# Kernel tuning notes

Measured on AMD Instinct MI355X. Metric: run time of the kernel, lower is better.

Reference implementation:

```python
import jax, jax.numpy as jnp
import numpy as np

N = 200000          # nodes
E = 800000          # edges (avg degree ~4, molecular graphs)
F_IN = 128          # dataset.num_node_features
HID = 32            # hidden_channels -> widths 32, 64, 128
N_TASKS = 128       # dataset.num_tasks
G = 8000            # number of graphs in the batch
EPS = 1e-5


def _glorot(key, shape):
    fan_in, fan_out = shape[0], shape[1]
    lim = np.sqrt(6.0 / (fan_in + fan_out)).astype(np.float32)
    return jax.random.uniform(key, shape, jnp.float32, -lim, lim)


def setup_inputs() -> dict:
    key = jax.random.key(0)
    ks = jax.random.split(key, 16)
    x = jax.random.normal(ks[0], (N, F_IN), jnp.float32)
    edge_index = jax.random.randint(ks[1], (2, E), 0, N, jnp.int64)
    batch = jnp.sort(jax.random.randint(ks[2], (N,), 0, G, jnp.int64))
    return {
        "x": x,
        "edge_index": edge_index,
        "batch": batch,
        "norm_w": jnp.ones((1,), jnp.float32),
        "norm_b": jnp.zeros((1,), jnp.float32),
        "W1": _glorot(ks[3], (F_IN, HID)),
        "b1": jnp.zeros((HID,), jnp.float32),
        "W2": _glorot(ks[4], (HID, 2 * HID)),
        "b2": jnp.zeros((2 * HID,), jnp.float32),
        "W3": _glorot(ks[5], (2 * HID, 4 * HID)),
        "b3": jnp.zeros((4 * HID,), jnp.float32),
        "lin1_W": _glorot(ks[6], (4 * HID, 256)),
        "lin1_b": jnp.zeros((256,), jnp.float32),
        "lin2_W": _glorot(ks[7], (256, N_TASKS)),
        "lin2_b": jnp.zeros((N_TASKS,), jnp.float32),
    }


def _instance_norm(x, batch, w, b):
    # PyG InstanceNorm: per-graph, per-channel mean / biased var, scalar affine.
    ones = jnp.ones((x.shape[0], 1), x.dtype)
    cnt = jnp.maximum(jax.ops.segment_sum(ones, batch, num_segments=G), 1.0)  # [G,1]
    mean = jax.ops.segment_sum(x, batch, num_segments=G) / cnt               # [G,C]
    var = jax.ops.segment_sum(x * x, batch, num_segments=G) / cnt - mean * mean
    xn = (x - mean[batch]) * jax.lax.rsqrt(var[batch] + EPS)
    return xn * w + b


def _gcn_conv(x, src, dst, dis, W, b):
    # GCNConv: h = xW; out_i = sum_j (d_i d_j)^{-1/2} h_j over A+I edges; + bias.
    h = x @ W
    msg = h[src] * (dis[src] * dis[dst])[:, None]          # [E, C] gather
    agg = jax.ops.segment_sum(msg, dst, num_segments=x.shape[0])
    agg = agg + h * (dis * dis)[:, None]                   # self-loop term
    return agg + b


def reference(x, edge_index, batch, norm_w, norm_b, W1, b1, W2, b2, W3, b3,
              lin1_W, lin1_b, lin2_W, lin2_b):
    src, dst = edge_index[0], edge_index[1]
    # degrees on A + I (all edge weights 1)
    deg = 1.0 + jax.ops.segment_sum(jnp.ones((E,), x.dtype), dst, num_segments=N)
    dis = jax.lax.rsqrt(deg)                                # deg >= 1, safe

    h = _instance_norm(x, batch, norm_w, norm_b)
    h = jax.nn.relu(_gcn_conv(h, src, dst, dis, W1, b1))
    h = jax.nn.relu(_gcn_conv(h, src, dst, dis, W2, b2))
    h = jax.nn.relu(_gcn_conv(h, src, dst, dis, W3, b3))

    # global_max_pool; empty graphs -> 0 (values are >=0 post-relu)
    pooled = jnp.maximum(jax.ops.segment_max(h, batch, num_segments=G), 0.0)

    out = jax.nn.relu(pooled @ lin1_W + lin1_b)
    return out @ lin2_W + lin2_b
```

## Files before the change

### kernel.cpp

```cpp
#include <hip/hip_runtime.h>
#include <hip/hip_bf16.h>
#include <stdint.h>

#define NN 200000
#define NE 800000
#define FIN 128
#define NG 8000
#define EPSV 1e-5f
#define NBS ((NN + 255) / 256)

typedef __attribute__((ext_vector_type(8))) short bf16x8;
typedef __attribute__((ext_vector_type(4))) float f32x4;

static __device__ __forceinline__ bf16x8 as_bf16x8(uint4 u) {
    union { uint4 u; bf16x8 v; } c; c.u = u; return c.v;
}

static __device__ __forceinline__ void u2f(uint4 v, float4& lo, float4& hi) {
    lo.x = __uint_as_float(v.x << 16); lo.y = __uint_as_float(v.x & 0xffff0000u);
    lo.z = __uint_as_float(v.y << 16); lo.w = __uint_as_float(v.y & 0xffff0000u);
    hi.x = __uint_as_float(v.z << 16); hi.y = __uint_as_float(v.z & 0xffff0000u);
    hi.z = __uint_as_float(v.w << 16); hi.w = __uint_as_float(v.w & 0xffff0000u);
}
static __device__ __forceinline__ unsigned int pk(float a, float b) {
    __hip_bfloat16 x = __float2bfloat16(a), y = __float2bfloat16(b);
    return (unsigned int)(*(unsigned short*)&x) | ((unsigned int)(*(unsigned short*)&y) << 16);
}

__global__ void k_cnt(const int* __restrict__ dst, int* __restrict__ cnt) {
    int e = blockIdx.x * 256 + threadIdx.x;
    if (e < NE) atomicAdd(&cnt[dst[e]], 1);
}

__global__ void k_blocksum(const int* __restrict__ cnt, int* __restrict__ bsum) {
    __shared__ int sh[256];
    int b = blockIdx.x, t = threadIdx.x;
    int idx = b * 256 + t;
    sh[t] = (idx < NN) ? cnt[idx] : 0;
    __syncthreads();
    for (int o = 128; o > 0; o >>= 1) {
        if (t < o) sh[t] += sh[t + o];
        __syncthreads();
    }
    if (t == 0) bsum[b] = sh[0];
}

__global__ __launch_bounds__(1024) void k_scanb(const int* __restrict__ bsum, int* __restrict__ bpre) {
    __shared__ int sh[1024];
    int t = threadIdx.x;
    int v = (t < NBS) ? bsum[t] : 0;
    sh[t] = v;
    __syncthreads();
    for (int o = 1; o < 1024; o <<= 1) {
        int add = (t >= o) ? sh[t - o] : 0;
        __syncthreads();
        sh[t] += add;
        __syncthreads();
    }
    if (t < NBS) bpre[t] = sh[t] - v;
}

__global__ void k_scanchunk(int* __restrict__ cnt, const int* __restrict__ bpre,
                            int* __restrict__ rowstart, int* __restrict__ cursor) {
    __shared__ int sh[256];
    int b = blockIdx.x, t = threadIdx.x;
    int idx = b * 256 + t;
    int v = (idx < NN) ? cnt[idx] : 0;
    sh[t] = v;
    __syncthreads();
    for (int o = 1; o < 256; o <<= 1) {
        int add = (t >= o) ? sh[t - o] : 0;
        __syncthreads();
        sh[t] += add;
        __syncthreads();
    }
    if (idx < NN) {
        int rs = bpre[b] + sh[t] - v;
        rowstart[idx] = rs;
        cursor[idx] = rs;
        ((float*)cnt)[idx] = rsqrtf(1.0f + (float)v);
    }
    if (idx == 0) rowstart[NN] = NE;
}

__global__ void k_fill(const int* __restrict__ src, const int* __restrict__ dst,
                       int* __restrict__ cursor, int* __restrict__ csr) {
    int e = blockIdx.x * 256 + threadIdx.x;
    if (e < NE) {
        int pos = atomicAdd(&cursor[dst[e]], 1);
        csr[pos] = src[e];
    }
}

__global__ void k_starts(const int* __restrict__ batch, int* __restrict__ startg) {
    int n = blockIdx.x * 256 + threadIdx.x;
    if (n >= NN) return;
    int b = batch[n];
    int prev = (n == 0) ? -1 : batch[n - 1];
    for (int g = prev + 1; g <= b; ++g) startg[g] = n;
    if (n == NN - 1) {
        for (int g = b + 1; g <= NG; ++g) startg[g] = NN;
    }
}

__global__ __launch_bounds__(256) void k_w3split(const float* __restrict__ W3,
                                                 unsigned short* __restrict__ whi,
                                                 unsigned short* __restrict__ wlo) {
    int i = blockIdx.x * 256 + threadIdx.x;
    if (i >= 64 * 128) return;
    int n = i >> 6, k = i & 63;
    float w = W3[k * 128 + n];
    __hip_bfloat16 h = __float2bfloat16(w);
    float hf = __bfloat162float(h);
    __hip_bfloat16 l = __float2bfloat16(w - hf);
    whi[n * 64 + k] = *(unsigned short*)&h;
    wlo[n * 64 + k] = *(unsigned short*)&l;
}

__global__ __launch_bounds__(256) void k_stats2(const float* __restrict__ x,
                                                const int* __restrict__ startg,
                                                const float* __restrict__ nw,
                                                const float* __restrict__ nb,
                                                float* __restrict__ scale,
                                                float* __restrict__ shift) {
    __shared__ float4 rsum[256], rsq[256];
    int g = blockIdx.x;
    int s = startg[g], e = startg[g + 1];
    if (s == e) return;
    int t = threadIdx.x;
    int slot = t >> 5, c4 = t & 31;
    const float4* x4 = (const float4*)x;
    float4 sum = {0.f, 0.f, 0.f, 0.f}, sq = {0.f, 0.f, 0.f, 0.f};
    for (int n = s + slot; n < e; n += 8) {
        float4 v = x4[n * 32 + c4];
        sum.x += v.x; sum.y += v.y; sum.z += v.z; sum.w += v.w;
        sq.x += v.x * v.x; sq.y += v.y * v.y; sq.z += v.z * v.z; sq.w += v.w * v.w;
    }
    rsum[slot * 32 + c4] = sum;
    rsq[slot * 32 + c4] = sq;
    __syncthreads();
    if (t < 32) {
        float4 S = rsum[t], Q = rsq[t];
#pragma unroll
        for (int sl = 1; sl < 8; ++sl) {
            float4 a = rsum[sl * 32 + t], b = rsq[sl * 32 + t];
            S.x += a.x; S.y += a.y; S.z += a.z; S.w += a.w;
            Q.x += b.x; Q.y += b.y; Q.z += b.z; Q.w += b.w;
        }
        float inv = 1.0f / (float)(e - s);
        float w = nw[0], b = nb[0];
        float4 sc, sh;
        {
            float m = S.x * inv, v = fmaxf(Q.x * inv - m * m, 0.f);
            float is = rsqrtf(v + EPSV); sc.x = is * w; sh.x = b - m * is * w;
        }
        {
            float m = S.y * inv, v = fmaxf(Q.y * inv - m * m, 0.f);
            float is = rsqrtf(v + EPSV); sc.y = is * w; sh.y = b - m * is * w;
        }
        {
            float m = S.z * inv, v = fmaxf(Q.z * inv - m * m, 0.f);
            float is = rsqrtf(v + EPSV); sc.z = is * w; sh.z = b - m * is * w;
        }
        {
            float m = S.w * inv, v = fmaxf(Q.w * inv - m * m, 0.f);
            float is = rsqrtf(v + EPSV); sc.w = is * w; sh.w = b - m * is * w;
        }
        ((float4*)scale)[g * 32 + t] = sc;
        ((float4*)shift)[g * 32 + t] = sh;
    }
}

__global__ __launch_bounds__(256) void k_conv1s(const float* __restrict__ x,
                                                const int* __restrict__ batch,
                                                const float* __restrict__ scale,
                                                const float* __restrict__ shift,
                                                const float* __restrict__ W1,
                                                const float* __restrict__ dis,
                                                float* __restrict__ p1) {
    __shared__ float4 sx4[64 * 33];
    int t = threadIdx.x;
    int base = blockIdx.x * 64;
    const float4* x4 = (const float4*)x;
    const float4* sc4 = (const float4*)scale;
    const float4* sh4 = (const float4*)shift;
    for (int i = t; i < 64 * 32; i += 256) {
        int nl = i >> 5, c4 = i & 31;
        int n = base + nl;
        int g = batch[n];
        float4 xv = x4[n * 32 + c4];
        float4 sc = sc4[g * 32 + c4];
        float4 sh = sh4[g * 32 + c4];
        float4 r;
        r.x = fmaf(xv.x, sc.x, sh.x);
        r.y = fmaf(xv.y, sc.y, sh.y);
        r.z = fmaf(xv.z, sc.z, sh.z);
        r.w = fmaf(xv.w, sc.w, sh.w);
        sx4[nl * 33 + c4] = r;
    }
    __syncthreads();
    int lane = t & 63;
    int kq = __builtin_amdgcn_readfirstlane(t >> 6) * 2;
    const float4* W4 = (const float4*)W1;
    const float4* arow = &sx4[lane * 33];
    float4 acc0 = {0.f, 0.f, 0.f, 0.f}, acc1 = {0.f, 0.f, 0.f, 0.f};
#pragma unroll 4
    for (int c4 = 0; c4 < 32; ++c4) {
        float4 a = arow[c4];
        int rb = c4 * 32 + kq;
        float4 wA0 = W4[rb +  0], wA1 = W4[rb +  1];
        float4 wB0 = W4[rb +  8], wB1 = W4[rb +  9];
        float4 wC0 = W4[rb + 16], wC1 = W4[rb + 17];
        float4 wD0 = W4[rb + 24], wD1 = W4[rb + 25];
        acc0.x += a.x * wA0.x + a.y * wB0.x + a.z * wC0.x + a.w * wD0.x;
        acc0.y += a.x * wA0.y + a.y * wB0.y + a.z * wC0.y + a.w * wD0.y;
        acc0.z += a.x * wA0.z + a.y * wB0.z + a.z * wC0.z + a.w * wD0.z;
        acc0.w += a.x * wA0.w + a.y * wB0.w + a.z * wC0.w + a.w * wD0.w;
        acc1.x += a.x * wA1.x + a.y * wB1.x + a.z * wC1.x + a.w * wD1.x;
        acc1.y += a.x * wA1.y + a.y * wB1.y + a.z * wC1.y + a.w * wD1.y;
        acc1.z += a.x * wA1.z + a.y * wB1.z + a.z * wC1.z + a.w * wD1.z;
        acc1.w += a.x * wA1.w + a.y * wB1.w + a.z * wC1.w + a.w * wD1.w;
    }
    int n = base + lane;
    float d = dis[n];
    float4 r0, r1;
    r0.x = acc0.x * d; r0.y = acc0.y * d; r0.z = acc0.z * d; r0.w = acc0.w * d;
    r1.x = acc1.x * d; r1.y = acc1.y * d; r1.z = acc1.z * d; r1.w = acc1.w * d;
    ((float4*)p1)[n * 8 + kq] = r0;
    ((float4*)p1)[n * 8 + kq + 1] = r1;
}

__global__ __launch_bounds__(256) void k_gather1(const float* __restrict__ p1,
                                                 const int* __restrict__ rowstart,
                                                 const int* __restrict__ csr,
                                                 const float* __restrict__ dis,
                                                 const float* __restrict__ b1,
                                                 float* __restrict__ p2) {
    int tid = blockIdx.x * 256 + threadIdx.x;
    int n = tid >> 3, c4 = tid & 7;
    const float4* p1_4 = (const float4*)p1;
    int s = rowstart[n], e = rowstart[n + 1];
    float4 agg = p1_4[n * 8 + c4];
    int j = s;
    for (; j + 1 < e; j += 2) {
        float4 v0 = p1_4[csr[j] * 8 + c4];
        float4 v1 = p1_4[csr[j + 1] * 8 + c4];
        agg.x += v0.x + v1.x; agg.y += v0.y + v1.y;
        agg.z += v0.z + v1.z; agg.w += v0.w + v1.w;
    }
    if (j < e) {
        float4 v = p1_4[csr[j] * 8 + c4];
        agg.x += v.x; agg.y += v.y; agg.z += v.z; agg.w += v.w;
    }
    float d = dis[n];
    float4 bb = ((const float4*)b1)[c4];
    float4 r;
    r.x = fmaxf(d * agg.x + bb.x, 0.f) * d;
    r.y = fmaxf(d * agg.y + bb.y, 0.f) * d;
    r.z = fmaxf(d * agg.z + bb.z, 0.f) * d;
    r.w = fmaxf(d * agg.w + bb.w, 0.f) * d;
    ((float4*)p2)[n * 8 + c4] = r;
}

__global__ __launch_bounds__(256) void k_conv2g(const float* __restrict__ p2,
                                                const int* __restrict__ rowstart,
                                                const int* __restrict__ csr,
                                                const float* __restrict__ dis,
                                                const float* __restrict__ W2,
                                                const float* __restrict__ b2v,
                                                __hip_bfloat16* __restrict__ p3h) {
    __shared__ float sW[32 * 64];
    __shared__ float4 spart[16 * 16];
    __shared__ float sa[16 * 32];
    int t = threadIdx.x;
    const float4* W4 = (const float4*)W2;
    for (int i = t; i < 32 * 64 / 4; i += 256) ((float4*)sW)[i] = W4[i];
    int base = blockIdx.x * 16;
    const float4* p2_4 = (const float4*)p2;
    {
        int node = t >> 4, c4 = t & 7, half = (t >> 3) & 1;
        int n = base + node;
        int s = rowstart[n], e = rowstart[n + 1];
        float4 agg = {0.f, 0.f, 0.f, 0.f};
        if (half == 0) {
            agg = p2_4[n * 8 + c4];
            for (int j = s; j < e; j += 2) {
                float4 v = p2_4[csr[j] * 8 + c4];
                agg.x += v.x; agg.y += v.y; agg.z += v.z; agg.w += v.w;
            }
        } else {
            for (int j = s + 1; j < e; j += 2) {
                float4 v = p2_4[csr[j] * 8 + c4];
                agg.x += v.x; agg.y += v.y; agg.z += v.z; agg.w += v.w;
            }
        }
        spart[node * 16 + half * 8 + c4] = agg;
    }
    __syncthreads();
    if (t < 128) {
        int nd = t >> 3, cc = t & 7;
        float4 a = spart[nd * 16 + cc], b = spart[nd * 16 + 8 + cc];
        float d = dis[base + nd];
        float4 r;
        r.x = d * (a.x + b.x); r.y = d * (a.y + b.y);
        r.z = d * (a.z + b.z); r.w = d * (a.w + b.w);
        ((float4*)sa)[nd * 8 + cc] = r;
    }
    __syncthreads();
    int k = t & 63, grp = t >> 6;
    float acc[4] = {0.f, 0.f, 0.f, 0.f};
    for (int c = 0; c < 32; ++c) {
        float w = sW[c * 64 + k];
#pragma unroll
        for (int q = 0; q < 4; ++q) acc[q] += sa[(grp * 4 + q) * 32 + c] * w;
    }
    float bb = b2v[k];
#pragma unroll
    for (int q = 0; q < 4; ++q) {
        int n = base + grp * 4 + q;
        float h = fmaxf(acc[q] + bb, 0.f);
        p3h[n * 64 + k] = __float2bfloat16(h * dis[n]);
    }
}

__global__ __launch_bounds__(256) void k_gather3(const __hip_bfloat16* __restrict__ p3h,
                                                 const int* __restrict__ rowstart,
                                                 const int* __restrict__ csr,
                                                 const float* __restrict__ dis,
                                                 __hip_bfloat16* __restrict__ a3h) {
    int tid = blockIdx.x * 256 + threadIdx.x;
    int n = tid >> 3, c8 = tid & 7;
    const uint4* p3q = (const uint4*)p3h;
    int s = rowstart[n], e = rowstart[n + 1];
    float4 alo, ahi;
    u2f(p3q[n * 8 + c8], alo, ahi);
    int j = s;
    for (; j + 1 < e; j += 2) {
        float4 l0, h0, l1, h1;
        u2f(p3q[csr[j] * 8 + c8], l0, h0);
        u2f(p3q[csr[j + 1] * 8 + c8], l1, h1);
        alo.x += l0.x + l1.x; alo.y += l0.y + l1.y;
        alo.z += l0.z + l1.z; alo.w += l0.w + l1.w;
        ahi.x += h0.x + h1.x; ahi.y += h0.y + h1.y;
        ahi.z += h0.z + h1.z; ahi.w += h0.w + h1.w;
    }
    if (j < e) {
        float4 l0, h0;
        u2f(p3q[csr[j] * 8 + c8], l0, h0);
        alo.x += l0.x; alo.y += l0.y; alo.z += l0.z; alo.w += l0.w;
        ahi.x += h0.x; ahi.y += h0.y; ahi.z += h0.z; ahi.w += h0.w;
    }
    float d = dis[n];
    uint4 o;
    o.x = pk(d * alo.x, d * alo.y);
    o.y = pk(d * alo.z, d * alo.w);
    o.z = pk(d * ahi.x, d * ahi.y);
    o.w = pk(d * ahi.z, d * ahi.w);
    ((uint4*)a3h)[n * 8 + c8] = o;
}

__global__ __launch_bounds__(256) void k_conv3m(const __hip_bfloat16* __restrict__ a3h,
                                                const unsigned short* __restrict__ w3hi,
                                                const unsigned short* __restrict__ w3lo,
                                                const float* __restrict__ b3v,
                                                const int* __restrict__ batch,
                                                unsigned int* __restrict__ pooled) {
    __shared__ uint4 sa[64 * 9];
    __shared__ float sp[64 * 132];
    __shared__ int sbatch[64];
    int t = threadIdx.x;
    int base = blockIdx.x * 64;
    if (t < 64) sbatch[t] = batch[base + t];
    const uint4* a3q = (const uint4*)a3h;
    for (int i = t; i < 64 * 8; i += 256) {
        sa[(i >> 3) * 9 + (i & 7)] = a3q[(size_t)base * 8 + i];
    }
    __syncthreads();
    int lane = t & 63, w = t >> 6;
    int h = lane >> 4;
    int cid = lane & 15;
    const uint4* WHq = (const uint4*)w3hi;
    const uint4* WLq = (const uint4*)w3lo;
    uint4 bh[2][2], bl[2][2];
#pragma unroll
    for (int nl = 0; nl < 2; ++nl) {
        int n = (w * 2 + nl) * 16 + cid;
#pragma unroll
        for (int kt = 0; kt < 2; ++kt) {
            bh[nl][kt] = WHq[n * 8 + kt * 4 + h];
            bl[nl][kt] = WLq[n * 8 + kt * 4 + h];
        }
    }
    f32x4 acc[2][4];
#pragma unroll
    for (int nl = 0; nl < 2; ++nl)
#pragma unroll
        for (int mi = 0; mi < 4; ++mi) acc[nl][mi] = {0.f, 0.f, 0.f, 0.f};
#pragma unroll
    for (int mi = 0; mi < 4; ++mi) {
        int arow = (mi * 16 + cid) * 9;
        bf16x8 a0 = as_bf16x8(sa[arow + h]);
        bf16x8 a1 = as_bf16x8(sa[arow + 4 + h]);
#pragma unroll
        for (int nl = 0; nl < 2; ++nl) {
            acc[nl][mi] = __builtin_amdgcn_mfma_f32_16x16x32_bf16(a0, as_bf16x8(bh[nl][0]), acc[nl][mi], 0, 0, 0);
            acc[nl][mi] = __builtin_amdgcn_mfma_f32_16x16x32_bf16(a1, as_bf16x8(bh[nl][1]), acc[nl][mi], 0, 0, 0);
            acc[nl][mi] = __builtin_amdgcn_mfma_f32_16x16x32_bf16(a0, as_bf16x8(bl[nl][0]), acc[nl][mi], 0, 0, 0);
            acc[nl][mi] = __builtin_amdgcn_mfma_f32_16x16x32_bf16(a1, as_bf16x8(bl[nl][1]), acc[nl][mi], 0, 0, 0);
        }
    }
#pragma unroll
    for (int nl = 0; nl < 2; ++nl) {
        int ch = (w * 2 + nl) * 16 + cid;
        float bb = b3v[ch];
#pragma unroll
        for (int mi = 0; mi < 4; ++mi) {
#pragma unroll
            for (int r = 0; r < 4; ++r) {
                int node_l = mi * 16 + h * 4 + r;
                sp[node_l * 132 + ch] = fmaxf(acc[nl][mi][r] + bb, 0.f);
            }
        }
    }
    __syncthreads();
    unsigned int* spool = (unsigned int*)sa;
    for (int i = t; i < 16 * 128; i += 256) spool[i] = 0u;
    __syncthreads();
    int g0 = sbatch[0], g63 = sbatch[63];
    int k4 = t & 31, n0 = (t >> 5) * 8;
    int curg = sbatch[n0];
    float4 cm = {0.f, 0.f, 0.f, 0.f};
#pragma unroll
    for (int ii = 0; ii < 8; ++ii) {
        int g = sbatch[n0 + ii];
        float4 hv = *(const float4*)&sp[(n0 + ii) * 132 + k4 * 4];
        if (g != curg) {
            int s = curg - g0 - 1;
            if (s >= 0 && curg < g63 && s < 16) {
                unsigned int* d = spool + s * 128 + k4 * 4;
                atomicMax(d + 0, __float_as_uint(cm.x));
                atomicMax(d + 1, __float_as_uint(cm.y));
                atomicMax(d + 2, __float_as_uint(cm.z));
                atomicMax(d + 3, __float_as_uint(cm.w));
            } else {
                unsigned int* d = pooled + curg * 128 + k4 * 4;
                atomicMax(d + 0, __float_as_uint(cm.x));
                atomicMax(d + 1, __float_as_uint(cm.y));
                atomicMax(d + 2, __float_as_uint(cm.z));
                atomicMax(d + 3, __float_as_uint(cm.w));
            }
            cm = {0.f, 0.f, 0.f, 0.f};
            curg = g;
        }
        cm.x = fmaxf(cm.x, hv.x);
        cm.y = fmaxf(cm.y, hv.y);
        cm.z = fmaxf(cm.z, hv.z);
        cm.w = fmaxf(cm.w, hv.w);
    }
    {
        int s = curg - g0 - 1;
        if (s >= 0 && curg < g63 && s < 16) {
            unsigned int* d = spool + s * 128 + k4 * 4;
            atomicMax(d + 0, __float_as_uint(cm.x));
            atomicMax(d + 1, __float_as_uint(cm.y));
            atomicMax(d + 2, __float_as_uint(cm.z));
            atomicMax(d + 3, __float_as_uint(cm.w));
        } else {
            unsigned int* d = pooled + curg * 128 + k4 * 4;
            atomicMax(d + 0, __float_as_uint(cm.x));
            atomicMax(d + 1, __float_as_uint(cm.y));
            atomicMax(d + 2, __float_as_uint(cm.z));
            atomicMax(d + 3, __float_as_uint(cm.w));
        }
    }
    __syncthreads();
    {
        int s = t >> 4;
        int g = g0 + 1 + s;
        if (g < g63) {
            int ch = (t & 15) * 8;
            const float* spf = (const float*)spool;
            float4 v0 = *(const float4*)&spf[s * 128 + ch];
            float4 v1 = *(const float4*)&spf[s * 128 + ch + 4];
            float4* pf = (float4*)pooled;
            pf[g * 32 + (ch >> 2)] = v0;
            pf[g * 32 + (ch >> 2) + 1] = v1;
        }
    }
}

__global__ __launch_bounds__(256) void k_head(const float* __restrict__ pooled,
                                              const float* __restrict__ W1v,
                                              const float* __restrict__ b1v,
                                              const float* __restrict__ W2v,
                                              const float* __restrict__ b2v,
                                              float* __restrict__ out) {
    __shared__ __align__(16) float sp[8 * 128];
    __shared__ __align__(16) float smid[8 * 256];
    __shared__ __align__(16) float sred[8 * 128];
    int t = threadIdx.x;
    int base = blockIdx.x * 8;
    const float4* po4 = (const float4*)pooled;
    for (int i = t; i < 8 * 32; i += 256) ((float4*)sp)[i] = po4[base * 32 + i];
    __syncthreads();
    {
        float acc[8];
#pragma unroll
        for (int gl = 0; gl < 8; ++gl) acc[gl] = 0.f;
        const float4* sp4 = (const float4*)sp;
        for (int c4 = 0; c4 < 32; ++c4) {
            float w0 = W1v[(c4 * 4 + 0) * 256 + t];
            float w1 = W1v[(c4 * 4 + 1) * 256 + t];
            float w2 = W1v[(c4 * 4 + 2) * 256 + t];
            float w3 = W1v[(c4 * 4 + 3) * 256 + t];
#pragma unroll
            for (int gl = 0; gl < 8; ++gl) {
                float4 a = sp4[gl * 32 + c4];
                acc[gl] += a.x * w0 + a.y * w1 + a.z * w2 + a.w * w3;
            }
        }
        float bb = b1v[t];
#pragma unroll
        for (int gl = 0; gl < 8; ++gl) smid[gl * 256 + t] = fmaxf(acc[gl] + bb, 0.f);
    }
    __syncthreads();
    int k = t & 127, half = t >> 7;
    float acc2[8];
#pragma unroll
    for (int gl = 0; gl < 8; ++gl) acc2[gl] = 0.f;
    {
        const float* Wc = W2v + half * 128 * 128;
        const float4* sm4 = (const float4*)smid;
        for (int c4 = 0; c4 < 32; ++c4) {
            float w0 = Wc[(c4 * 4 + 0) * 128 + k];
            float w1 = Wc[(c4 * 4 + 1) * 128 + k];
            float w2 = Wc[(c4 * 4 + 2) * 128 + k];
            float w3 = Wc[(c4 * 4 + 3) * 128 + k];
#pragma unroll
            for (int gl = 0; gl < 8; ++gl) {
                float4 a = sm4[gl * 64 + half * 32 + c4];
                acc2[gl] += a.x * w0 + a.y * w1 + a.z * w2 + a.w * w3;
            }
        }
    }
    if (half == 1) {
#pragma unroll
        for (int gl = 0; gl < 8; ++gl) sred[gl * 128 + k] = acc2[gl];
    }
    __syncthreads();
    if (half == 0) {
        float bb = b2v[k];
#pragma unroll
        for (int gl = 0; gl < 8; ++gl)
            out[(base + gl) * 128 + k] = acc2[gl] + sred[gl * 128 + k] + bb;
    }
}

extern "C" void kernel_launch(void* const* d_in, const int* in_sizes, int n_in,
                              void* d_out, int out_size, void* d_ws, size_t ws_size,
                              hipStream_t stream) {
    (void)in_sizes; (void)n_in; (void)out_size; (void)ws_size;
    const float* x   = (const float*)d_in[0];
    const int* ei    = (const int*)d_in[1];
    const int* src = ei;
    const int* dst = ei + NE;
    const int* batch = (const int*)d_in[2];
    const float* nw  = (const float*)d_in[3];
    const float* nb  = (const float*)d_in[4];
    const float* W1  = (const float*)d_in[5];
    const float* b1  = (const float*)d_in[6];
    const float* W2  = (const float*)d_in[7];
    const float* b2  = (const float*)d_in[8];
    const float* W3  = (const float*)d_in[9];
    const float* b3  = (const float*)d_in[10];
    const float* l1W = (const float*)d_in[11];
    const float* l1b = (const float*)d_in[12];
    const float* l2W = (const float*)d_in[13];
    const float* l2b = (const float*)d_in[14];
    float* out = (float*)d_out;

    char* wsp = (char*)d_ws;
    int*   cnt      = (int*)wsp;   wsp += (size_t)NN * 4;
    int*   rowstart = (int*)wsp;   wsp += (size_t)(NN + 1) * 4;
    int*   cursor   = (int*)wsp;   wsp += (size_t)NN * 4;
    int*   bsum     = (int*)wsp;   wsp += (size_t)NBS * 4;
    int*   bpre     = (int*)wsp;   wsp += (size_t)NBS * 4;
    int*   startg   = (int*)wsp;   wsp += (size_t)(NG + 1) * 4;
    int*   csr      = (int*)wsp;   wsp += (size_t)NE * 4;
    wsp += ((256 - ((uintptr_t)wsp & 255)) & 255);
    unsigned short* w3hi = (unsigned short*)wsp; wsp += (size_t)128 * 64 * 2;
    unsigned short* w3lo = (unsigned short*)wsp; wsp += (size_t)128 * 64 * 2;
    float* scale   = (float*)wsp; wsp += (size_t)NG * 128 * 4;
    float* shift   = (float*)wsp; wsp += (size_t)NG * 128 * 4;
    float* pooled  = (float*)wsp; wsp += (size_t)NG * 128 * 4;
    float* regionA = (float*)wsp; wsp += (size_t)NN * 64 * 4;
    float* regionB = (float*)wsp; wsp += (size_t)NN * 64 * 4;

    float* dis  = (float*)cnt;
    float* p1   = regionA;
    float* p2   = regionA + (size_t)NN * 32;
    __hip_bfloat16* p3h = (__hip_bfloat16*)regionB;
    __hip_bfloat16* a3h = (__hip_bfloat16*)regionA;

    hipMemsetAsync(cnt, 0, (size_t)NN * 4, stream);
    k_cnt<<<(NE + 255) / 256, 256, 0, stream>>>(dst, cnt);
    k_blocksum<<<NBS, 256, 0, stream>>>(cnt, bsum);
    k_scanb<<<1, 1024, 0, stream>>>(bsum, bpre);
    k_scanchunk<<<NBS, 256, 0, stream>>>(cnt, bpre, rowstart, cursor);
    k_fill<<<(NE + 255) / 256, 256, 0, stream>>>(src, dst, cursor, csr);
    k_w3split<<<32, 256, 0, stream>>>(W3, w3hi, w3lo);

    k_starts<<<(NN + 255) / 256, 256, 0, stream>>>(batch, startg);
    k_stats2<<<NG, 256, 0, stream>>>(x, startg, nw, nb, scale, shift);
    k_conv1s<<<NN / 64, 256, 0, stream>>>(x, batch, scale, shift, W1, dis, p1);
    k_gather1<<<NN * 8 / 256, 256, 0, stream>>>(p1, rowstart, csr, dis, b1, p2);
    k_conv2g<<<NN / 16, 256, 0, stream>>>(p2, rowstart, csr, dis, W2, b2, p3h);
    k_gather3<<<NN * 8 / 256, 256, 0, stream>>>(p3h, rowstart, csr, dis, a3h);
    hipMemsetAsync(pooled, 0, (size_t)NG * 128 * 4, stream);
    k_conv3m<<<NN / 64, 256, 0, stream>>>(a3h, w3hi, w3lo, b3, batch, (unsigned int*)pooled);

    k_head<<<NG / 8, 256, 0, stream>>>(pooled, l1W, l1b, l2W, l2b, out);
}
```

Before: 488.8 us.

## Merge prep kernels and fuse layer-3 gather into the MFMA conv kernel

Independent setup kernels (edge degree count, graph start offsets, W3 hi/lo split) are merged into one launch, and the CSR fill is merged with the instance-norm statistics kernel using block-index dispatch. The layer-3 neighbor gather now runs inside the conv3 MFMA kernel and writes aggregated bf16 rows straight into shared memory, which removes the a3h intermediate round trip and two launches. The trade-off is that conv3's load phase now carries irregular gather latency with only 64 rows per block, and the merged kernels mix workloads of very different shapes.

New measurement: 481.8 us. About the same (-1.4%).

```diff
diff --git a/kernel.cpp b/kernel.cpp
--- a/kernel.cpp
+++ b/kernel.cpp
@@ -8,6 +8,7 @@
 #define NG 8000
 #define EPSV 1e-5f
 #define NBS ((NN + 255) / 256)
+#define CNT_B (NE / 256)
 
 typedef __attribute__((ext_vector_type(8))) short bf16x8;
 typedef __attribute__((ext_vector_type(4))) float f32x4;
@@ -27,9 +28,35 @@
     return (unsigned int)(*(unsigned short*)&x) | ((unsigned int)(*(unsigned short*)&y) << 16);
 }
 
-__global__ void k_cnt(const int* __restrict__ dst, int* __restrict__ cnt) {
-    int e = blockIdx.x * 256 + threadIdx.x;
-    if (e < NE) atomicAdd(&cnt[dst[e]], 1);
+__global__ __launch_bounds__(256) void k_prep1(const int* __restrict__ dst, int* __restrict__ cnt,
+                                               const int* __restrict__ batch, int* __restrict__ startg,
+                                               const float* __restrict__ W3,
+                                               unsigned short* __restrict__ whi,
+                                               unsigned short* __restrict__ wlo) {
+    int b = blockIdx.x, t = threadIdx.x;
+    if (b < CNT_B) {
+        int e = b * 256 + t;
+        atomicAdd(&cnt[dst[e]], 1);
+    } else if (b < CNT_B + NBS) {
+        int n = (b - CNT_B) * 256 + t;
+        if (n >= NN) return;
+        int bb = batch[n];
+        int prev = (n == 0) ? -1 : batch[n - 1];
+        for (int g = prev + 1; g <= bb; ++g) startg[g] = n;
+        if (n == NN - 1) {
+            for (int g = bb + 1; g <= NG; ++g) startg[g] = NN;
+        }
+    } else {
+        int i = (b - CNT_B - NBS) * 256 + t;
+        if (i >= 64 * 128) return;
+        int n = i >> 6, k = i & 63;
+        float w = W3[k * 128 + n];
+        __hip_bfloat16 h = __float2bfloat16(w);
+        float hf = __bfloat162float(h);
+        __hip_bfloat16 l = __float2bfloat16(w - hf);
+        whi[n * 64 + k] = *(unsigned short*)&h;
+        wlo[n * 64 + k] = *(unsigned short*)&l;
+    }
 }
 
 __global__ void k_blocksum(const int* __restrict__ cnt, int* __restrict__ bsum) {
@@ -83,51 +110,25 @@
     if (idx == 0) rowstart[NN] = NE;
 }
 
-__global__ void k_fill(const int* __restrict__ src, const int* __restrict__ dst,
-                       int* __restrict__ cursor, int* __restrict__ csr) {
-    int e = blockIdx.x * 256 + threadIdx.x;
-    if (e < NE) {
+__global__ __launch_bounds__(256) void k_prep2(const int* __restrict__ src, const int* __restrict__ dst,
+                                               int* __restrict__ cursor, int* __restrict__ csr,
+                                               const float* __restrict__ x,
+                                               const int* __restrict__ startg,
+                                               const float* __restrict__ nw,
+                                               const float* __restrict__ nb,
+                                               float* __restrict__ scale,
+                                               float* __restrict__ shift) {
+    __shared__ float4 rsum[256], rsq[256];
+    int b = blockIdx.x, t = threadIdx.x;
+    if (b < CNT_B) {
+        int e = b * 256 + t;
         int pos = atomicAdd(&cursor[dst[e]], 1);
         csr[pos] = src[e];
-    }
-}
-
-__global__ void k_starts(const int* __restrict__ batch, int* __restrict__ startg) {
-    int n = blockIdx.x * 256 + threadIdx.x;
-    if (n >= NN) return;
-    int b = batch[n];
-    int prev = (n == 0) ? -1 : batch[n - 1];
-    for (int g = prev + 1; g <= b; ++g) startg[g] = n;
-    if (n == NN - 1) {
-        for (int g = b + 1; g <= NG; ++g) startg[g] = NN;
-    }
-}
-
-__global__ __launch_bounds__(256) void k_w3split(const float* __restrict__ W3,
-                                                 unsigned short* __restrict__ whi,
-                                                 unsigned short* __restrict__ wlo) {
-    int i = blockIdx.x * 256 + threadIdx.x;
-    if (i >= 64 * 128) return;
-    int n = i >> 6, k = i & 63;
-    float w = W3[k * 128 + n];
-    __hip_bfloat16 h = __float2bfloat16(w);
-    float hf = __bfloat162float(h);
-    __hip_bfloat16 l = __float2bfloat16(w - hf);
-    whi[n * 64 + k] = *(unsigned short*)&h;
-    wlo[n * 64 + k] = *(unsigned short*)&l;
-}
-
-__global__ __launch_bounds__(256) void k_stats2(const float* __restrict__ x,
-                                                const int* __restrict__ startg,
-                                                const float* __restrict__ nw,
-                                                const float* __restrict__ nb,
-                                                float* __restrict__ scale,
-                                                float* __restrict__ shift) {
-    __shared__ float4 rsum[256], rsq[256];
-    int g = blockIdx.x;
+        return;
+    }
+    int g = b - CNT_B;
     int s = startg[g], e = startg[g + 1];
     if (s == e) return;
-    int t = threadIdx.x;
     int slot = t >> 5, c4 = t & 31;
     const float4* x4 = (const float4*)x;
     float4 sum = {0.f, 0.f, 0.f, 0.f}, sq = {0.f, 0.f, 0.f, 0.f};
@@ -143,28 +144,28 @@
         float4 S = rsum[t], Q = rsq[t];
 #pragma unroll
         for (int sl = 1; sl < 8; ++sl) {
-            float4 a = rsum[sl * 32 + t], b = rsq[sl * 32 + t];
+            float4 a = rsum[sl * 32 + t], bq = rsq[sl * 32 + t];
             S.x += a.x; S.y += a.y; S.z += a.z; S.w += a.w;
-            Q.x += b.x; Q.y += b.y; Q.z += b.z; Q.w += b.w;
+            Q.x += bq.x; Q.y += bq.y; Q.z += bq.z; Q.w += bq.w;
         }
         float inv = 1.0f / (float)(e - s);
-        float w = nw[0], b = nb[0];
+        float w = nw[0], bb = nb[0];
         float4 sc, sh;
         {
             float m = S.x * inv, v = fmaxf(Q.x * inv - m * m, 0.f);
-            float is = rsqrtf(v + EPSV); sc.x = is * w; sh.x = b - m * is * w;
+            float is = rsqrtf(v + EPSV); sc.x = is * w; sh.x = bb - m * is * w;
         }
         {
             float m = S.y * inv, v = fmaxf(Q.y * inv - m * m, 0.f);
-            float is = rsqrtf(v + EPSV); sc.y = is * w; sh.y = b - m * is * w;
+            float is = rsqrtf(v + EPSV); sc.y = is * w; sh.y = bb - m * is * w;
         }
         {
             float m = S.z * inv, v = fmaxf(Q.z * inv - m * m, 0.f);
-            float is = rsqrtf(v + EPSV); sc.z = is * w; sh.z = b - m * is * w;
+            float is = rsqrtf(v + EPSV); sc.z = is * w; sh.z = bb - m * is * w;
         }
         {
             float m = S.w * inv, v = fmaxf(Q.w * inv - m * m, 0.f);
-            float is = rsqrtf(v + EPSV); sc.w = is * w; sh.w = b - m * is * w;
+            float is = rsqrtf(v + EPSV); sc.w = is * w; sh.w = bb - m * is * w;
         }
         ((float4*)scale)[g * 32 + t] = sc;
         ((float4*)shift)[g * 32 + t] = sh;
@@ -323,57 +324,51 @@
     }
 }
 
-__global__ __launch_bounds__(256) void k_gather3(const __hip_bfloat16* __restrict__ p3h,
+__global__ __launch_bounds__(256) void k_conv3mg(const __hip_bfloat16* __restrict__ p3h,
                                                  const int* __restrict__ rowstart,
                                                  const int* __restrict__ csr,
                                                  const float* __restrict__ dis,
-                                                 __hip_bfloat16* __restrict__ a3h) {
-    int tid = blockIdx.x * 256 + threadIdx.x;
-    int n = tid >> 3, c8 = tid & 7;
-    const uint4* p3q = (const uint4*)p3h;
-    int s = rowstart[n], e = rowstart[n + 1];
-    float4 alo, ahi;
-    u2f(p3q[n * 8 + c8], alo, ahi);
-    int j = s;
-    for (; j + 1 < e; j += 2) {
-        float4 l0, h0, l1, h1;
-        u2f(p3q[csr[j] * 8 + c8], l0, h0);
-        u2f(p3q[csr[j + 1] * 8 + c8], l1, h1);
-        alo.x += l0.x + l1.x; alo.y += l0.y + l1.y;
-        alo.z += l0.z + l1.z; alo.w += l0.w + l1.w;
-        ahi.x += h0.x + h1.x; ahi.y += h0.y + h1.y;
-        ahi.z += h0.z + h1.z; ahi.w += h0.w + h1.w;
-    }
-    if (j < e) {
-        float4 l0, h0;
-        u2f(p3q[csr[j] * 8 + c8], l0, h0);
-        alo.x += l0.x; alo.y += l0.y; alo.z += l0.z; alo.w += l0.w;
-        ahi.x += h0.x; ahi.y += h0.y; ahi.z += h0.z; ahi.w += h0.w;
-    }
-    float d = dis[n];
-    uint4 o;
-    o.x = pk(d * alo.x, d * alo.y);
-    o.y = pk(d * alo.z, d * alo.w);
-    o.z = pk(d * ahi.x, d * ahi.y);
-    o.w = pk(d * ahi.z, d * ahi.w);
-    ((uint4*)a3h)[n * 8 + c8] = o;
-}
-
-__global__ __launch_bounds__(256) void k_conv3m(const __hip_bfloat16* __restrict__ a3h,
-                                                const unsigned short* __restrict__ w3hi,
-                                                const unsigned short* __restrict__ w3lo,
-                                                const float* __restrict__ b3v,
-                                                const int* __restrict__ batch,
-                                                unsigned int* __restrict__ pooled) {
+                                                 const unsigned short* __restrict__ w3hi,
+                                                 const unsigned short* __restrict__ w3lo,
+                                                 const float* __restrict__ b3v,
+                                                 const int* __restrict__ batch,
+                                                 unsigned int* __restrict__ pooled) {
     __shared__ uint4 sa[64 * 9];
     __shared__ float sp[64 * 132];
     __shared__ int sbatch[64];
     int t = threadIdx.x;
     int base = blockIdx.x * 64;
     if (t < 64) sbatch[t] = batch[base + t];
-    const uint4* a3q = (const uint4*)a3h;
+    const uint4* p3q = (const uint4*)p3h;
     for (int i = t; i < 64 * 8; i += 256) {
-        sa[(i >> 3) * 9 + (i & 7)] = a3q[(size_t)base * 8 + i];
+        int nl = i >> 3, c8 = i & 7;
+        int n = base + nl;
+        int s = rowstart[n], e = rowstart[n + 1];
+        float4 alo, ahi;
+        u2f(p3q[n * 8 + c8], alo, ahi);
+        int j = s;
+        for (; j + 1 < e; j += 2) {
+            float4 l0, h0, l1, h1;
+            u2f(p3q[csr[j] * 8 + c8], l0, h0);
+            u2f(p3q[csr[j + 1] * 8 + c8], l1, h1);
+            alo.x += l0.x + l1.x; alo.y += l0.y + l1.y;
+            alo.z += l0.z + l1.z; alo.w += l0.w + l1.w;
+            ahi.x += h0.x + h1.x; ahi.y += h0.y + h1.y;
+            ahi.z += h0.z + h1.z; ahi.w += h0.w + h1.w;
+        }
+        if (j < e) {
+            float4 l0, h0;
+            u2f(p3q[csr[j] * 8 + c8], l0, h0);
+            alo.x += l0.x; alo.y += l0.y; alo.z += l0.z; alo.w += l0.w;
+            ahi.x += h0.x; ahi.y += h0.y; ahi.z += h0.z; ahi.w += h0.w;
+        }
+        float d = dis[n];
+        uint4 o;
+        o.x = pk(d * alo.x, d * alo.y);
+        o.y = pk(d * alo.z, d * alo.w);
+        o.z = pk(d * ahi.x, d * ahi.y);
+        o.w = pk(d * ahi.z, d * ahi.w);
+        sa[nl * 9 + c8] = o;
     }
     __syncthreads();
     int lane = t & 63, w = t >> 6;
@@ -600,24 +595,20 @@
     float* p1   = regionA;
     float* p2   = regionA + (size_t)NN * 32;
     __hip_bfloat16* p3h = (__hip_bfloat16*)regionB;
-    __hip_bfloat16* a3h = (__hip_bfloat16*)regionA;
 
     hipMemsetAsync(cnt, 0, (size_t)NN * 4, stream);
-    k_cnt<<<(NE + 255) / 256, 256, 0, stream>>>(dst, cnt);
+    k_prep1<<<CNT_B + NBS + 32, 256, 0, stream>>>(dst, cnt, batch, startg, W3, w3hi, w3lo);
     k_blocksum<<<NBS, 256, 0, stream>>>(cnt, bsum);
     k_scanb<<<1, 1024, 0, stream>>>(bsum, bpre);
     k_scanchunk<<<NBS, 256, 0, stream>>>(cnt, bpre, rowstart, cursor);
-    k_fill<<<(NE + 255) / 256, 256, 0, stream>>>(src, dst, cursor, csr);
-    k_w3split<<<32, 256, 0, stream>>>(W3, w3hi, w3lo);
-
-    k_starts<<<(NN + 255) / 256, 256, 0, stream>>>(batch, startg);
-    k_stats2<<<NG, 256, 0, stream>>>(x, startg, nw, nb, scale, shift);
+    k_prep2<<<CNT_B + NG, 256, 0, stream>>>(src, dst, cursor, csr, x, startg, nw, nb, scale, shift);
+
     k_conv1s<<<NN / 64, 256, 0, stream>>>(x, batch, scale, shift, W1, dis, p1);
     k_gather1<<<NN * 8 / 256, 256, 0, stream>>>(p1, rowstart, csr, dis, b1, p2);
     k_conv2g<<<NN / 16, 256, 0, stream>>>(p2, rowstart, csr, dis, W2, b2, p3h);
-    k_gather3<<<NN * 8 / 256, 256, 0, stream>>>(p3h, rowstart, csr, dis, a3h);
     hipMemsetAsync(pooled, 0, (size_t)NG * 128 * 4, stream);
-    k_conv3m<<<NN / 64, 256, 0, stream>>>(a3h, w3hi, w3lo, b3, batch, (unsigned int*)pooled);
+    k_conv3mg<<<NN / 64, 256, 0, stream>>>(p3h, rowstart, csr, dis, w3hi, w3lo, b3, batch,
+                                           (unsigned int*)pooled);
 
     k_head<<<NG / 8, 256, 0, stream>>>(pooled, l1W, l1b, l2W, l2b, out);
 }
```
